# Optimization experiments

Hardware: AMD Instinct MI355X
Metric: run time of the kernel (lower is better)

Reference implementation:

```python
import jax, jax.numpy as jnp
import numpy as np

B, N, C = 8, 4096, 64          # graphs, points per graph, feature dim
RATIO = 0.25
M = int(N * RATIO)             # 1024 sampled centroids per graph
R = 0.2                        # radius (points live in the unit cube)
K = 64                         # max_num_neighbors in the forward
BIG = 1e10


def fps_single(pos):
    """Farthest point sampling on one cloud. pos: [N,3] -> [M] local indices.
    Deterministic start at index 0 (PyG uses a random start; math is identical)."""
    n = pos.shape[0]

    def step(carry, _):
        mind, last = carry
        d = jnp.sum((pos - pos[last]) ** 2, axis=-1)      # [N]
        mind = jnp.minimum(mind, d)
        nxt = jnp.argmax(mind)
        return (mind, nxt), nxt

    init = (jnp.full((n,), BIG, pos.dtype), jnp.int32(0))
    _, rest = jax.lax.scan(step, init, None, length=M - 1)
    return jnp.concatenate([jnp.zeros((1,), rest.dtype), rest])


def setup_inputs() -> dict:
    key = jax.random.key(0)
    ks = jax.random.split(key, 8)
    x = jax.random.normal(ks[0], (B * N, C), dtype=jnp.float32)
    pos = jax.random.uniform(ks[1], (B * N, 3), dtype=jnp.float32)
    batch = jnp.repeat(jnp.arange(B, dtype=jnp.int64), N)
    seed_idx = jnp.arange(B * N, dtype=jnp.int64)
    d_in, h, f_out = C + 3, 128, 256
    W1 = jax.random.normal(ks[2], (d_in, h), dtype=jnp.float32) / np.sqrt(d_in)
    b1 = jnp.zeros((h,), jnp.float32)
    W2 = jax.random.normal(ks[3], (h, h), dtype=jnp.float32) / np.sqrt(h)
    b2 = jnp.zeros((h,), jnp.float32)
    W3 = jax.random.normal(ks[4], (h, f_out), dtype=jnp.float32) / np.sqrt(h)
    b3 = jnp.zeros((f_out,), jnp.float32)
    return {"x": x, "pos": pos, "batch": batch, "seed_idx": seed_idx,
            "W1": W1, "b1": b1, "W2": W2, "b2": b2, "W3": W3, "b3": b3}


def reference(x, pos, batch, seed_idx, W1, b1, W2, b2, W3, b3):
    posb = pos.reshape(B, N, 3)
    xb = x.reshape(B, N, C)

    # --- FPS per graph (batch is block-contiguous with N points per graph) ---
    idx_local = jax.vmap(fps_single)(posb)                     # [B, M]
    ctr = jax.vmap(lambda p, i: p[i])(posb, idx_local)         # [B, M, 3]

    # --- radius neighbor search: up to K neighbors within r of each centroid ---
    d2 = jnp.sum((ctr[:, :, None, :] - posb[:, None, :, :]) ** 2, axis=-1)  # [B,M,N]
    d2m = jnp.where(d2 < R * R, d2, BIG)
    neg_d, nbr = jax.lax.top_k(-d2m, K)                        # K nearest within r
    valid = (-neg_d) < R * R                                   # [B, M, K]

    # --- PointConv: msg = MLP([x_j, pos_j - pos_i]), max-aggregate ---
    x_j = jax.vmap(lambda a, i: a[i])(xb, nbr)                 # [B, M, K, C]
    pos_j = jax.vmap(lambda p, i: p[i])(posb, nbr)             # [B, M, K, 3]
    msg = jnp.concatenate([x_j, pos_j - ctr[:, :, None, :]], axis=-1)  # [B,M,K,C+3]
    h = jax.nn.relu(msg @ W1 + b1)
    h = jax.nn.relu(h @ W2 + b2)
    h = jax.nn.relu(h @ W3 + b3)                               # [B, M, K, 256]
    h = jnp.where(valid[..., None], h, -BIG)
    out = jnp.max(h, axis=2)                                   # [B, M, 256]
    out = jnp.where(jnp.any(valid, axis=-1)[..., None], out, 0.0)

    # --- gather sampled outputs back to the flat layout ---
    idx_flat = (idx_local + jnp.arange(B)[:, None] * N).reshape(-1)  # [B*M]
    x_out = out.reshape(B * M, -1)
    pos_out = pos[idx_flat]
    batch_out = batch[idx_flat]
    seed_out = seed_idx[idx_flat]
    return x_out, pos_out, batch_out, seed_out
```

## Files before the change

### kernel.cpp

```cpp
#include <hip/hip_runtime.h>
#include <stdint.h>

#define BB 8
#define NN 4096
#define CC 64
#define MM 1024
#define EE (BB*MM)
#define KK 64
#define F3 256
#define SM 104
#define SH 136
#define CAP 768

typedef __bf16 bf16x8 __attribute__((ext_vector_type(8)));
typedef float floatx4 __attribute__((ext_vector_type(4)));

#define DPP_MAXSTEP(ctrl, rmask) { \
    unsigned o = (unsigned)__builtin_amdgcn_update_dpp(0, (int)v, ctrl, rmask, 0xf, false); \
    v = v > o ? v : o; }
__device__ __forceinline__ unsigned wave_umax_u32(unsigned v) {
  DPP_MAXSTEP(0x111, 0xf)
  DPP_MAXSTEP(0x112, 0xf)
  DPP_MAXSTEP(0x114, 0xf)
  DPP_MAXSTEP(0x118, 0xf)
  DPP_MAXSTEP(0x142, 0xa)
  DPP_MAXSTEP(0x143, 0xc)
  return (unsigned)__builtin_amdgcn_readlane((int)v, 63);
}
#define DPP_MINSTEP(ctrl, rmask) { \
    unsigned o = (unsigned)__builtin_amdgcn_update_dpp((int)0xffffffffu, (int)v, ctrl, rmask, 0xf, false); \
    v = v < o ? v : o; }
__device__ __forceinline__ unsigned wave_umin_u32(unsigned v) {
  DPP_MINSTEP(0x111, 0xf)
  DPP_MINSTEP(0x112, 0xf)
  DPP_MINSTEP(0x114, 0xf)
  DPP_MINSTEP(0x118, 0xf)
  DPP_MINSTEP(0x142, 0xa)
  DPP_MINSTEP(0x143, 0xc)
  return (unsigned)__builtin_amdgcn_readlane((int)v, 63);
}

__global__ __launch_bounds__(512) void fps_prep_kernel(
    const float* __restrict__ pos,
    const float* __restrict__ W1, const float* __restrict__ W2, const float* __restrict__ W3,
    int* __restrict__ fpsIdx, float* __restrict__ ctr,
    __bf16* __restrict__ W1t, __bf16* __restrict__ W2t, __bf16* __restrict__ W3t,
    float4* __restrict__ pos4) {
  __shared__ float4 sP4[NN];
  __shared__ unsigned long long sRed[2][8];
  const int blk = blockIdx.x;
  const int t = threadIdx.x;

  if (blk >= BB) {
    if (blk < 128) {
      const int i0 = (blk - 8) * 512 + t;
      if (i0 < 128 * 96) {
        const int n = i0 / 96, k = i0 % 96;
        W1t[i0] = (k < 67) ? (__bf16)W1[k * 128 + n] : (__bf16)0.0f;
      } else if (i0 < 128 * 96 + 128 * 128) {
        const int i = i0 - 128 * 96;
        const int n = i / 128, k = i % 128;
        W2t[i] = (__bf16)W2[k * 128 + n];
      } else {
        const int i = i0 - (128 * 96 + 128 * 128);
        const int n = i / 128, k = i % 128;
        W3t[i] = (__bf16)W3[k * 256 + n];
      }
    } else {
      const int i = (blk - 128) * 512 + t;
      pos4[i] = make_float4(pos[(long)i * 3 + 0], pos[(long)i * 3 + 1],
                            pos[(long)i * 3 + 2], 0.0f);
    }
    return;
  }

  const int g = blk;
  const int lane = t & 63, wv = t >> 6;
  float px[8], py[8], pz[8], mind[8];
#pragma unroll
  for (int j = 0; j < 8; ++j) {
    const int p = t + (j << 9);
    const long base = ((long)g * NN + p) * 3;
    px[j] = pos[base + 0];
    py[j] = pos[base + 1];
    pz[j] = pos[base + 2];
    mind[j] = 1e10f;
    sP4[p] = make_float4(px[j], py[j], pz[j], 0.0f);
  }
  __syncthreads();
  float wx = sP4[0].x, wy = sP4[0].y, wz = sP4[0].z;
  int win0 = 0, win1 = 0;
  for (int s = 1; s < MM; ++s) {
    unsigned bb = 0u, bidx = (unsigned)t;
#pragma unroll
    for (int j = 0; j < 8; ++j) {
      const float dx = __fsub_rn(px[j], wx);
      const float dy = __fsub_rn(py[j], wy);
      const float dz = __fsub_rn(pz[j], wz);
      const float d2 = __fadd_rn(__fadd_rn(__fmul_rn(dx, dx), __fmul_rn(dy, dy)), __fmul_rn(dz, dz));
      mind[j] = fminf(mind[j], d2);
      const unsigned mb = __float_as_uint(mind[j]);
      if (mb > bb) { bb = mb; bidx = (unsigned)(t + (j << 9)); }
    }
    const unsigned maxv = wave_umax_u32(bb);
    const unsigned cand = (bb == maxv) ? bidx : 0xffffffffu;
    const unsigned minidx = wave_umin_u32(cand);
    if (lane == 0)
      sRed[s & 1][wv] = ((unsigned long long)maxv << 32) | (unsigned long long)(~minidx);
    __syncthreads();
    unsigned long long m = sRed[s & 1][0];
#pragma unroll
    for (int w = 1; w < 8; ++w) {
      const unsigned long long o = sRed[s & 1][w];
      m = o > m ? o : m;
    }
    const int widx = (int)(~(unsigned)m);
    const float4 wp = sP4[widx];
    wx = wp.x; wy = wp.y; wz = wp.z;
    if (s == t)       win0 = widx;
    if (s == t + 512) win1 = widx;
  }
  {
    const long e0 = (long)g * MM + t;
    const float4 p0 = sP4[win0];
    fpsIdx[e0] = win0;
    ctr[e0 * 3 + 0] = p0.x; ctr[e0 * 3 + 1] = p0.y; ctr[e0 * 3 + 2] = p0.z;
    const long e1 = e0 + 512;
    const float4 p1 = sP4[win1];
    fpsIdx[e1] = win1;
    ctr[e1 * 3 + 0] = p1.x; ctr[e1 * 3 + 1] = p1.y; ctr[e1 * 3 + 2] = p1.z;
  }
}

__global__ __launch_bounds__(512) void mlp_kernel(const float* __restrict__ x,
    const float4* __restrict__ pos4, const float* __restrict__ ctr,
    const int* __restrict__ fpsIdx,
    const __bf16* __restrict__ W1t, const __bf16* __restrict__ W2t,
    const __bf16* __restrict__ W3t,
    const float* __restrict__ b1, const float* __restrict__ b2,
    const float* __restrict__ b3,
    float* __restrict__ outX, float* __restrict__ outP,
    float* __restrict__ outB, float* __restrict__ outS) {
  __shared__ __align__(16) __bf16 sMsg[64 * SM];
  __shared__ __align__(16) __bf16 sH[64 * SH];
  __shared__ int sSel[KK];
  __shared__ int sCnt;
  unsigned long long* sDI = (unsigned long long*)sMsg;

  const int e = blockIdx.x;
  const int t = threadIdx.x;
  const int b = e >> 10;
  const int lane = t & 63, wv = t >> 6;

  if (t == 0) sCnt = 0;
  const float cx = ctr[(long)e * 3 + 0];
  const float cy = ctr[(long)e * 3 + 1];
  const float cz = ctr[(long)e * 3 + 2];
  if (t < 3) outP[(long)e * 3 + t] = ctr[(long)e * 3 + t];
  if (t == 3) { outB[e] = (float)b; outS[e] = (float)(b * NN + fpsIdx[e]); }
  const float R2 = (float)(0.2 * 0.2);
  __syncthreads();

#pragma unroll
  for (int q = 0; q < NN / 512; ++q) {
    const int p = t + q * 512;
    const float4 P = pos4[b * NN + p];
    const float dx = __fsub_rn(cx, P.x);
    const float dy = __fsub_rn(cy, P.y);
    const float dz = __fsub_rn(cz, P.z);
    const float d2 = __fadd_rn(__fadd_rn(__fmul_rn(dx, dx), __fmul_rn(dy, dy)), __fmul_rn(dz, dz));
    const bool v = d2 < R2;
    const unsigned long long mask = __ballot(v);
    int wbase = 0;
    if (lane == 0 && mask) wbase = atomicAdd(&sCnt, (int)__popcll(mask));
    wbase = __shfl(wbase, 0);
    if (v) {
      const int off = wbase + (int)__popcll(mask & ((1ull << lane) - 1ull));
      if (off < CAP)
        sDI[off] = ((unsigned long long)__float_as_uint(d2) << 32) | (unsigned)p;
    }
  }
  __syncthreads();
  int cnt = sCnt; cnt = cnt > CAP ? CAP : cnt;
  const int nsel = cnt < KK ? cnt : KK;

  for (int i = t; i < cnt; i += 512) {
    const unsigned long long my = sDI[i];
    int rank = 0;
#pragma unroll 8
    for (int j = 0; j < cnt; ++j) rank += (sDI[j] < my) ? 1 : 0;
    if (rank < KK) sSel[rank] = (int)(unsigned)(my & 0xffffffffu);
  }
  __syncthreads();
  cnt = nsel;

  {
    const int r = t >> 3, p = t & 7;
    float4 a = make_float4(0.f, 0.f, 0.f, 0.f), c4 = a;
    if (r < cnt) {
      const float* xr = x + (long)(b * NN + sSel[r]) * CC + p * 8;
      a  = *(const float4*)xr;
      c4 = *(const float4*)(xr + 4);
    }
    __bf16 o[8] = {(__bf16)a.x, (__bf16)a.y, (__bf16)a.z, (__bf16)a.w,
                   (__bf16)c4.x, (__bf16)c4.y, (__bf16)c4.z, (__bf16)c4.w};
    *(uint4*)&sMsg[r * SM + p * 8] = *(uint4*)o;
  }
  if (t < 64) {
    const int r = t;
    __bf16 d0 = (__bf16)0.0f, d1 = (__bf16)0.0f, d2v = (__bf16)0.0f;
    if (r < cnt) {
      const float4 P = pos4[b * NN + sSel[r]];
      d0  = (__bf16)__fsub_rn(P.x, cx);
      d1  = (__bf16)__fsub_rn(P.y, cy);
      d2v = (__bf16)__fsub_rn(P.z, cz);
    }
    sMsg[r * SM + 64] = d0;
    sMsg[r * SM + 65] = d1;
    sMsg[r * SM + 66] = d2v;
    for (int c = 67; c < SM; ++c) sMsg[r * SM + c] = (__bf16)0.0f;
  }
  __syncthreads();

  const int l15 = lane & 15, quad = lane >> 4;
  {
    floatx4 acc[4] = {};
    const __bf16* wrow = W1t + (wv * 16 + l15) * 96;
#pragma unroll
    for (int ks = 0; ks < 3; ++ks) {
      const bf16x8 bfrag = *(const bf16x8*)(wrow + ks * 32 + quad * 8);
#pragma unroll
      for (int mt = 0; mt < 4; ++mt) {
        const bf16x8 afrag = *(const bf16x8*)&sMsg[(mt * 16 + l15) * SM + ks * 32 + quad * 8];
        acc[mt] = __builtin_amdgcn_mfma_f32_16x16x32_bf16(afrag, bfrag, acc[mt], 0, 0, 0);
      }
    }
    const int col = wv * 16 + l15;
    const float bias = b1[col];
#pragma unroll
    for (int mt = 0; mt < 4; ++mt)
#pragma unroll
      for (int rg = 0; rg < 4; ++rg) {
        const int row = mt * 16 + quad * 4 + rg;
        float v = acc[mt][rg] + bias;
        v = v > 0.0f ? v : 0.0f;
        sH[row * SH + col] = (__bf16)v;
      }
  }
  __syncthreads();
  {
    floatx4 acc[4] = {};
    const __bf16* wrow = W2t + (wv * 16 + l15) * 128;
#pragma unroll
    for (int ks = 0; ks < 4; ++ks) {
      const bf16x8 bfrag = *(const bf16x8*)(wrow + ks * 32 + quad * 8);
#pragma unroll
      for (int mt = 0; mt < 4; ++mt) {
        const bf16x8 afrag = *(const bf16x8*)&sH[(mt * 16 + l15) * SH + ks * 32 + quad * 8];
        acc[mt] = __builtin_amdgcn_mfma_f32_16x16x32_bf16(afrag, bfrag, acc[mt], 0, 0, 0);
      }
    }
    __syncthreads();
    const int col = wv * 16 + l15;
    const float bias = b2[col];
#pragma unroll
    for (int mt = 0; mt < 4; ++mt)
#pragma unroll
      for (int rg = 0; rg < 4; ++rg) {
        const int row = mt * 16 + quad * 4 + rg;
        float v = acc[mt][rg] + bias;
        v = v > 0.0f ? v : 0.0f;
        sH[row * SH + col] = (__bf16)v;
      }
  }
  __syncthreads();
  {
    floatx4 acc[2][4] = {};
#pragma unroll
    for (int ks = 0; ks < 4; ++ks) {
      bf16x8 afrag[4];
#pragma unroll
      for (int mt = 0; mt < 4; ++mt)
        afrag[mt] = *(const bf16x8*)&sH[(mt * 16 + l15) * SH + ks * 32 + quad * 8];
#pragma unroll
      for (int i = 0; i < 2; ++i) {
        const bf16x8 bfrag = *(const bf16x8*)(W3t + ((wv * 2 + i) * 16 + l15) * 128 + ks * 32 + quad * 8);
#pragma unroll
        for (int mt = 0; mt < 4; ++mt)
          acc[i][mt] = __builtin_amdgcn_mfma_f32_16x16x32_bf16(afrag[mt], bfrag, acc[i][mt], 0, 0, 0);
      }
    }
#pragma unroll
    for (int i = 0; i < 2; ++i) {
      const int col = (wv * 2 + i) * 16 + l15;
      const float bias = b3[col];
      float mx = 0.0f;
#pragma unroll
      for (int mt = 0; mt < 4; ++mt)
#pragma unroll
        for (int rg = 0; rg < 4; ++rg) {
          const int row = mt * 16 + quad * 4 + rg;
          float v = acc[i][mt][rg] + bias;
          v = v > 0.0f ? v : 0.0f;
          if (row < cnt) mx = fmaxf(mx, v);
        }
      mx = fmaxf(mx, __shfl_xor(mx, 16));
      mx = fmaxf(mx, __shfl_xor(mx, 32));
      if (quad == 0) outX[(long)e * F3 + col] = mx;
    }
  }
}

extern "C" void kernel_launch(void* const* d_in, const int* in_sizes, int n_in,
                              void* d_out, int out_size, void* d_ws, size_t ws_size,
                              hipStream_t stream) {
  const float* x   = (const float*)d_in[0];
  const float* pos = (const float*)d_in[1];
  const float* W1  = (const float*)d_in[4];
  const float* b1  = (const float*)d_in[5];
  const float* W2  = (const float*)d_in[6];
  const float* b2  = (const float*)d_in[7];
  const float* W3  = (const float*)d_in[8];
  const float* b3  = (const float*)d_in[9];

  char* ws = (char*)d_ws;
  int*    fpsIdx = (int*)(ws);
  float*  ctr    = (float*)(ws + 32768);
  __bf16* W1t    = (__bf16*)(ws + 131072);
  __bf16* W2t    = (__bf16*)(ws + 155648);
  __bf16* W3t    = (__bf16*)(ws + 188416);
  float4* pos4   = (float4*)(ws + 253952);

  float* outX = (float*)d_out;
  float* outP = outX + (long)EE * F3;
  float* outB = outP + (long)EE * 3;
  float* outS = outB + EE;

  fps_prep_kernel<<<192, 512, 0, stream>>>(pos, W1, W2, W3,
                                           fpsIdx, ctr, W1t, W2t, W3t, pos4);
  mlp_kernel<<<EE, 512, 0, stream>>>(x, pos4, ctr, fpsIdx, W1t, W2t, W3t,
                                     b1, b2, b3, outX, outP, outB, outS);
}
```

Baseline: 861.8 us.

## Process two FPS graphs per block with 256 threads to share barriers

```diff
diff --git a/kernel.cpp b/kernel.cpp
--- a/kernel.cpp
+++ b/kernel.cpp
@@ -40,20 +40,20 @@
   return (unsigned)__builtin_amdgcn_readlane((int)v, 63);
 }
 
-__global__ __launch_bounds__(512) void fps_prep_kernel(
+__global__ __launch_bounds__(256, 1) void fps_prep_kernel(
     const float* __restrict__ pos,
     const float* __restrict__ W1, const float* __restrict__ W2, const float* __restrict__ W3,
     int* __restrict__ fpsIdx, float* __restrict__ ctr,
     __bf16* __restrict__ W1t, __bf16* __restrict__ W2t, __bf16* __restrict__ W3t,
     float4* __restrict__ pos4) {
-  __shared__ float4 sP4[NN];
-  __shared__ unsigned long long sRed[2][8];
+  __shared__ float4 sP4[2][NN];
+  __shared__ unsigned long long sRed[2][2][4];
   const int blk = blockIdx.x;
   const int t = threadIdx.x;
 
-  if (blk >= BB) {
-    if (blk < 128) {
-      const int i0 = (blk - 8) * 512 + t;
+  if (blk >= 4) {
+    if (blk < 244) {
+      const int i0 = (blk - 4) * 256 + t;
       if (i0 < 128 * 96) {
         const int n = i0 / 96, k = i0 % 96;
         W1t[i0] = (k < 67) ? (__bf16)W1[k * 128 + n] : (__bf16)0.0f;
@@ -67,68 +67,122 @@
         W3t[i] = (__bf16)W3[k * 256 + n];
       }
     } else {
-      const int i = (blk - 128) * 512 + t;
+      const int i = (blk - 244) * 256 + t;
       pos4[i] = make_float4(pos[(long)i * 3 + 0], pos[(long)i * 3 + 1],
                             pos[(long)i * 3 + 2], 0.0f);
     }
     return;
   }
 
-  const int g = blk;
+  const int gA = blk * 2, gB = gA + 1;
   const int lane = t & 63, wv = t >> 6;
-  float px[8], py[8], pz[8], mind[8];
-#pragma unroll
-  for (int j = 0; j < 8; ++j) {
-    const int p = t + (j << 9);
-    const long base = ((long)g * NN + p) * 3;
-    px[j] = pos[base + 0];
-    py[j] = pos[base + 1];
-    pz[j] = pos[base + 2];
-    mind[j] = 1e10f;
-    sP4[p] = make_float4(px[j], py[j], pz[j], 0.0f);
-  }
-  __syncthreads();
-  float wx = sP4[0].x, wy = sP4[0].y, wz = sP4[0].z;
-  int win0 = 0, win1 = 0;
+  float pxA[16], pyA[16], pzA[16], mindA[16];
+  float pxB[16], pyB[16], pzB[16], mindB[16];
+#pragma unroll
+  for (int j = 0; j < 16; ++j) {
+    const int p = t + (j << 8);
+    {
+      const long base = ((long)gA * NN + p) * 3;
+      pxA[j] = pos[base + 0]; pyA[j] = pos[base + 1]; pzA[j] = pos[base + 2];
+      mindA[j] = 1e10f;
+      sP4[0][p] = make_float4(pxA[j], pyA[j], pzA[j], 0.0f);
+    }
+    {
+      const long base = ((long)gB * NN + p) * 3;
+      pxB[j] = pos[base + 0]; pyB[j] = pos[base + 1]; pzB[j] = pos[base + 2];
+      mindB[j] = 1e10f;
+      sP4[1][p] = make_float4(pxB[j], pyB[j], pzB[j], 0.0f);
+    }
+  }
+  __syncthreads();
+  float wxA, wyA, wzA, wxB, wyB, wzB;
+  { const float4 w0 = sP4[0][0]; wxA = w0.x; wyA = w0.y; wzA = w0.z; }
+  { const float4 w0 = sP4[1][0]; wxB = w0.x; wyB = w0.y; wzB = w0.z; }
+  int winA0 = 0, winA1 = 0, winA2 = 0, winA3 = 0;
+  int winB0 = 0, winB1 = 0, winB2 = 0, winB3 = 0;
   for (int s = 1; s < MM; ++s) {
-    unsigned bb = 0u, bidx = (unsigned)t;
-#pragma unroll
-    for (int j = 0; j < 8; ++j) {
-      const float dx = __fsub_rn(px[j], wx);
-      const float dy = __fsub_rn(py[j], wy);
-      const float dz = __fsub_rn(pz[j], wz);
+    unsigned bbA = 0u, bidxA = (unsigned)t;
+#pragma unroll
+    for (int j = 0; j < 16; ++j) {
+      const float dx = __fsub_rn(pxA[j], wxA);
+      const float dy = __fsub_rn(pyA[j], wyA);
+      const float dz = __fsub_rn(pzA[j], wzA);
       const float d2 = __fadd_rn(__fadd_rn(__fmul_rn(dx, dx), __fmul_rn(dy, dy)), __fmul_rn(dz, dz));
-      mind[j] = fminf(mind[j], d2);
-      const unsigned mb = __float_as_uint(mind[j]);
-      if (mb > bb) { bb = mb; bidx = (unsigned)(t + (j << 9)); }
-    }
-    const unsigned maxv = wave_umax_u32(bb);
-    const unsigned cand = (bb == maxv) ? bidx : 0xffffffffu;
-    const unsigned minidx = wave_umin_u32(cand);
-    if (lane == 0)
-      sRed[s & 1][wv] = ((unsigned long long)maxv << 32) | (unsigned long long)(~minidx);
+      mindA[j] = fminf(mindA[j], d2);
+      const unsigned mb = __float_as_uint(mindA[j]);
+      if (mb > bbA) { bbA = mb; bidxA = (unsigned)(t + (j << 8)); }
+    }
+    unsigned bbB = 0u, bidxB = (unsigned)t;
+#pragma unroll
+    for (int j = 0; j < 16; ++j) {
+      const float dx = __fsub_rn(pxB[j], wxB);
+      const float dy = __fsub_rn(pyB[j], wyB);
+      const float dz = __fsub_rn(pzB[j], wzB);
+      const float d2 = __fadd_rn(__fadd_rn(__fmul_rn(dx, dx), __fmul_rn(dy, dy)), __fmul_rn(dz, dz));
+      mindB[j] = fminf(mindB[j], d2);
+      const unsigned mb = __float_as_uint(mindB[j]);
+      if (mb > bbB) { bbB = mb; bidxB = (unsigned)(t + (j << 8)); }
+    }
+    const unsigned maxvA = wave_umax_u32(bbA);
+    const unsigned maxvB = wave_umax_u32(bbB);
+    const unsigned widxA = wave_umin_u32((bbA == maxvA) ? bidxA : 0xffffffffu);
+    const unsigned widxB = wave_umin_u32((bbB == maxvB) ? bidxB : 0xffffffffu);
+    if (lane == 0) {
+      sRed[0][s & 1][wv] = ((unsigned long long)maxvA << 32) | (unsigned long long)(~widxA);
+      sRed[1][s & 1][wv] = ((unsigned long long)maxvB << 32) | (unsigned long long)(~widxB);
+    }
     __syncthreads();
-    unsigned long long m = sRed[s & 1][0];
-#pragma unroll
-    for (int w = 1; w < 8; ++w) {
-      const unsigned long long o = sRed[s & 1][w];
-      m = o > m ? o : m;
-    }
-    const int widx = (int)(~(unsigned)m);
-    const float4 wp = sP4[widx];
-    wx = wp.x; wy = wp.y; wz = wp.z;
-    if (s == t)       win0 = widx;
-    if (s == t + 512) win1 = widx;
-  }
-  {
-    const long e0 = (long)g * MM + t;
-    const float4 p0 = sP4[win0];
-    fpsIdx[e0] = win0;
-    ctr[e0 * 3 + 0] = p0.x; ctr[e0 * 3 + 1] = p0.y; ctr[e0 * 3 + 2] = p0.z;
-    const long e1 = e0 + 512;
-    const float4 p1 = sP4[win1];
-    fpsIdx[e1] = win1;
-    ctr[e1 * 3 + 0] = p1.x; ctr[e1 * 3 + 1] = p1.y; ctr[e1 * 3 + 2] = p1.z;
+    unsigned long long mA = sRed[0][s & 1][0];
+    unsigned long long mB = sRed[1][s & 1][0];
+#pragma unroll
+    for (int w = 1; w < 4; ++w) {
+      const unsigned long long oA = sRed[0][s & 1][w];
+      const unsigned long long oB = sRed[1][s & 1][w];
+      mA = oA > mA ? oA : mA;
+      mB = oB > mB ? oB : mB;
+    }
+    const int wiA = (int)(~(unsigned)mA);
+    const int wiB = (int)(~(unsigned)mB);
+    const float4 wpA = sP4[0][wiA];
+    const float4 wpB = sP4[1][wiB];
+    wxA = wpA.x; wyA = wpA.y; wzA = wpA.z;
+    wxB = wpB.x; wyB = wpB.y; wzB = wpB.z;
+    winA0 = (s == t)       ? wiA : winA0;
+    winA1 = (s == t + 256) ? wiA : winA1;
+    winA2 = (s == t + 512) ? wiA : winA2;
+    winA3 = (s == t + 768) ? wiA : winA3;
+    winB0 = (s == t)       ? wiB : winB0;
+    winB1 = (s == t + 256) ? wiB : winB1;
+    winB2 = (s == t + 512) ? wiB : winB2;
+    winB3 = (s == t + 768) ? wiB : winB3;
+  }
+  {
+    const long eA = (long)gA * MM + t;
+    const float4 a0 = sP4[0][winA0];
+    fpsIdx[eA] = winA0;
+    ctr[eA * 3 + 0] = a0.x; ctr[eA * 3 + 1] = a0.y; ctr[eA * 3 + 2] = a0.z;
+    const float4 a1 = sP4[0][winA1];
+    fpsIdx[eA + 256] = winA1;
+    ctr[(eA + 256) * 3 + 0] = a1.x; ctr[(eA + 256) * 3 + 1] = a1.y; ctr[(eA + 256) * 3 + 2] = a1.z;
+    const float4 a2 = sP4[0][winA2];
+    fpsIdx[eA + 512] = winA2;
+    ctr[(eA + 512) * 3 + 0] = a2.x; ctr[(eA + 512) * 3 + 1] = a2.y; ctr[(eA + 512) * 3 + 2] = a2.z;
+    const float4 a3 = sP4[0][winA3];
+    fpsIdx[eA + 768] = winA3;
+    ctr[(eA + 768) * 3 + 0] = a3.x; ctr[(eA + 768) * 3 + 1] = a3.y; ctr[(eA + 768) * 3 + 2] = a3.z;
+    const long eB = (long)gB * MM + t;
+    const float4 b0 = sP4[1][winB0];
+    fpsIdx[eB] = winB0;
+    ctr[eB * 3 + 0] = b0.x; ctr[eB * 3 + 1] = b0.y; ctr[eB * 3 + 2] = b0.z;
+    const float4 b1v = sP4[1][winB1];
+    fpsIdx[eB + 256] = winB1;
+    ctr[(eB + 256) * 3 + 0] = b1v.x; ctr[(eB + 256) * 3 + 1] = b1v.y; ctr[(eB + 256) * 3 + 2] = b1v.z;
+    const float4 b2v = sP4[1][winB2];
+    fpsIdx[eB + 512] = winB2;
+    ctr[(eB + 512) * 3 + 0] = b2v.x; ctr[(eB + 512) * 3 + 1] = b2v.y; ctr[(eB + 512) * 3 + 2] = b2v.z;
+    const float4 b3v = sP4[1][winB3];
+    fpsIdx[eB + 768] = winB3;
+    ctr[(eB + 768) * 3 + 0] = b3v.x; ctr[(eB + 768) * 3 + 1] = b3v.y; ctr[(eB + 768) * 3 + 2] = b3v.z;
   }
 }
 
@@ -336,7 +390,7 @@
   float* outB = outP + (long)EE * 3;
   float* outS = outB + EE;
 
-  fps_prep_kernel<<<192, 512, 0, stream>>>(pos, W1, W2, W3,
+  fps_prep_kernel<<<372, 256, 0, stream>>>(pos, W1, W2, W3,
                                            fpsIdx, ctr, W1t, W2t, W3t, pos4);
   mlp_kernel<<<EE, 512, 0, stream>>>(x, pos4, ctr, fpsIdx, W1t, W2t, W3t,
                                      b1, b2, b3, outX, outP, outB, outS);
```

Result: slower. 1.171 ms (+35.9%).
